# Optimization experiments

Hardware: AMD Instinct MI355X
Metric: run time of the kernel (lower is better)

Reference implementation:

```python
import jax, jax.numpy as jnp
import numpy as np

B, N, F_IN, F_OUT = 32, 1024, 64, 64
ALPHA = 0.2  # LeakyReLU negative slope


def setup_inputs() -> dict:
    key = jax.random.key(0)
    k1, k2, k3, k4 = jax.random.split(key, 4)
    node_features = jax.random.normal(k1, (B, N, F_IN), dtype=jnp.float32)
    adjacency = jax.random.uniform(k2, (B, N, N)) > 0.5
    adjacency = adjacency | jnp.eye(N, dtype=bool)[None]  # self-loops: no all-masked row
    # xavier_uniform-scale params (normal with matching std is fine for a reference)
    W = jax.random.normal(k3, (F_IN, F_OUT), dtype=jnp.float32) * (2.0 / (F_IN + F_OUT)) ** 0.5
    a = jax.random.normal(k4, (2 * F_OUT, 1), dtype=jnp.float32) * (2.0 / (2 * F_OUT + 1)) ** 0.5
    return {"node_features": node_features, "adjacency": adjacency, "W": W, "a": a}


def reference(node_features, adjacency, W, a):
    # h = X W : (B, N, F_OUT)
    h = node_features @ W
    # a^T [h_i || h_j] = h_i . a1 + h_j . a2  (exact decomposition of the concat score)
    a1 = a[:F_OUT, 0]
    a2 = a[F_OUT:, 0]
    f1 = jnp.einsum('bnf,f->bn', h, a1)  # (B, N)
    f2 = jnp.einsum('bnf,f->bn', h, a2)  # (B, N)
    e = jax.nn.leaky_relu(f1[:, :, None] + f2[:, None, :], negative_slope=ALPHA)  # (B,N,N)
    e = jnp.where(adjacency, e, -jnp.inf)
    attention = jax.nn.softmax(e, axis=-1)  # masked softmax over neighbors j
    h_prime = jnp.einsum('bij,bjf->bif', attention, h)  # (B, N, F_OUT)
    return jax.nn.elu(h_prime)  # concat=True branch
```

## Files before the change

kernel.cpp:

```cpp
#include <hip/hip_runtime.h>
#include <hip/hip_bf16.h>


#define B_  32
#define N_  1024
#define F_  64

typedef __attribute__((ext_vector_type(8))) short  short8;
typedef __attribute__((ext_vector_type(4))) float  floatx4;

__device__ __forceinline__ short f2bf(float x) {
    unsigned u = __float_as_uint(x);
    u += 0x7fff + ((u >> 16) & 1);
    return (short)(u >> 16);
}

__global__ __launch_bounds__(256) void gat_prep(
    const float* __restrict__ nf, const float* __restrict__ W, const float* __restrict__ a,
    float* __restrict__ f1, float* __restrict__ f2, short* __restrict__ h_swz)
{
    const int wave = threadIdx.x >> 6;
    const int lane = threadIdx.x & 63;
    const long long row0 = (long long)blockIdx.x * 16 + wave * 4;

    const float* nf0 = nf + row0 * F_;
    float acc0 = 0.f, acc1 = 0.f, acc2 = 0.f, acc3 = 0.f;
    #pragma unroll 8
    for (int k = 0; k < F_; ++k) {
        float wk = W[k * F_ + lane];
        acc0 = fmaf(nf0[k],          wk, acc0);
        acc1 = fmaf(nf0[F_ + k],     wk, acc1);
        acc2 = fmaf(nf0[2 * F_ + k], wk, acc2);
        acc3 = fmaf(nf0[3 * F_ + k], wk, acc3);
    }
    const float a1 = a[lane], a2 = a[F_ + lane];

    float accs[4] = {acc0, acc1, acc2, acc3};
    #pragma unroll
    for (int r = 0; r < 4; ++r) {
        float v  = accs[r];
        float s1 = v * a1, s2 = v * a2;
        #pragma unroll
        for (int off = 32; off >= 1; off >>= 1) {
            s1 += __shfl_xor(s1, off, 64);
            s2 += __shfl_xor(s2, off, 64);
        }
        long long row = row0 + r;
        if (lane == 0) { f1[row] = s1; f2[row] = s2; }
        int jl = (int)(row & (N_ - 1));
        int k  = jl & 31;
        int n  = lane & 15, fg = lane >> 4;
        int lp = n | ((k >> 3) << 4), e = k & 7;
        long long gc = row >> 5;
        h_swz[(gc * 4 + fg) * 512 + lp * 8 + e] = f2bf(v);
    }
}

__global__ __launch_bounds__(256) void gat_attn(
    const int* __restrict__ adj, const float* __restrict__ f1g, const float* __restrict__ f2g,
    const short* __restrict__ h_swz, float* __restrict__ out)
{
    const int wave = threadIdx.x >> 6;
    const int lane = threadIdx.x & 63;
    const int b  = blockIdx.x >> 4;
    const int ib = blockIdx.x & 15;
    const int i_base = ib * 64 + wave * 16;
    const int iw = lane & 15;
    const int kg = lane >> 4;
    const int i  = i_base + iw;

    const float f1i = f1g[b * N_ + i];
    const int*   adjrow = adj + ((long long)b * N_ + i) * N_ + kg * 8;
    const float* f2b    = f2g + b * N_ + kg * 8;
    const short* hb     = h_swz + (long long)b * 65536 + lane * 8;

    floatx4 acc0 = {0.f,0.f,0.f,0.f}, acc1 = {0.f,0.f,0.f,0.f};
    floatx4 acc2 = {0.f,0.f,0.f,0.f}, acc3 = {0.f,0.f,0.f,0.f};
    float s_lane = 0.f;

    for (int jc = 0; jc < 32; ++jc) {
        int4 aA = *(const int4*)(adjrow + jc * 32);
        int4 aB = *(const int4*)(adjrow + jc * 32 + 4);
        floatx4 fA = *(const floatx4*)(f2b + jc * 32);
        floatx4 fB = *(const floatx4*)(f2b + jc * 32 + 4);

        int   am[8] = {aA.x, aA.y, aA.z, aA.w, aB.x, aB.y, aB.z, aB.w};
        float fv[8] = {fA[0], fA[1], fA[2], fA[3], fB[0], fB[1], fB[2], fB[3]};

        short8 afrag;
        #pragma unroll
        for (int e = 0; e < 8; ++e) {
            float x  = f1i + fv[e];
            x        = fmaxf(x, 0.2f * x);
            float pe = am[e] ? __expf(x) : 0.f;
            s_lane  += pe;
            afrag[e] = f2bf(pe);
        }

        const short* hc = hb + jc * 2048;
        short8 b0 = *(const short8*)(hc);
        short8 b1 = *(const short8*)(hc + 512);
        short8 b2 = *(const short8*)(hc + 1024);
        short8 b3 = *(const short8*)(hc + 1536);

        acc0 = __builtin_amdgcn_mfma_f32_16x16x32_bf16(afrag, b0, acc0, 0, 0, 0);
        acc1 = __builtin_amdgcn_mfma_f32_16x16x32_bf16(afrag, b1, acc1, 0, 0, 0);
        acc2 = __builtin_amdgcn_mfma_f32_16x16x32_bf16(afrag, b2, acc2, 0, 0, 0);
        acc3 = __builtin_amdgcn_mfma_f32_16x16x32_bf16(afrag, b3, acc3, 0, 0, 0);
    }

    s_lane += __shfl_xor(s_lane, 16, 64);
    s_lane += __shfl_xor(s_lane, 32, 64);

    float* orow = out + ((long long)b * N_ + i_base) * F_;
    floatx4 accs[4] = {acc0, acc1, acc2, acc3};
    #pragma unroll
    for (int fg = 0; fg < 4; ++fg) {
        #pragma unroll
        for (int r = 0; r < 4; ++r) {
            int rloc = kg * 4 + r;
            float sr = __shfl(s_lane, rloc, 64);
            float v  = accs[fg][r] / sr;
            v = v > 0.f ? v : (__expf(v) - 1.f);
            orow[(long long)rloc * F_ + fg * 16 + iw] = v;
        }
    }
}

extern "C" void kernel_launch(void* const* d_in, const int* in_sizes, int n_in,
                              void* d_out, int out_size, void* d_ws, size_t ws_size,
                              hipStream_t stream) {
    const float* nf  = (const float*)d_in[0];
    const int*   adj = (const int*)d_in[1];
    const float* W   = (const float*)d_in[2];
    const float* a   = (const float*)d_in[3];
    float* out = (float*)d_out;

    char* ws = (char*)d_ws;
    float* f1    = (float*)ws;
    float* f2    = (float*)(ws + 131072);
    short* h_swz = (short*)(ws + 262144);

    hipLaunchKernelGGL(gat_prep, dim3(B_ * N_ / 16), dim3(256), 0, stream,
                       nf, W, a, f1, f2, h_swz);
    hipLaunchKernelGGL(gat_attn, dim3(B_ * (N_ / 64)), dim3(256), 0, stream,
                       adj, f1, f2, h_swz, out);
}
```

Baseline: 58.53 us.

## Split attention j-range across waves with shared-memory reduction of partial sums

Each block now handles 16 rows instead of 64, and its four waves each cover a quarter of the neighbor dimension. Partial MFMA accumulators and row sums go to LDS and are combined after a barrier, with each wave finishing one feature group. The grid grows fourfold to 2048 blocks, so more waves are in flight to hide latency on the adjacency stream. In exchange it adds LDS traffic and a __syncthreads, and the loads are reordered with an occupancy hint in the launch bounds.

```diff
diff --git a/kernel.cpp b/kernel.cpp
--- a/kernel.cpp
+++ b/kernel.cpp
@@ -56,52 +56,67 @@
     }
 }
 
-__global__ __launch_bounds__(256) void gat_attn(
+__global__ __launch_bounds__(256, 8) void gat_attn(
     const int* __restrict__ adj, const float* __restrict__ f1g, const float* __restrict__ f2g,
     const short* __restrict__ h_swz, float* __restrict__ out)
 {
+    __shared__ float part[4][64][17];
+    __shared__ float srow[4][16];
+
     const int wave = threadIdx.x >> 6;
     const int lane = threadIdx.x & 63;
-    const int b  = blockIdx.x >> 4;
-    const int ib = blockIdx.x & 15;
-    const int i_base = ib * 64 + wave * 16;
+    const int b  = blockIdx.x >> 6;
+    const int ig = blockIdx.x & 63;
+    const int i_base = ig * 16;
     const int iw = lane & 15;
     const int kg = lane >> 4;
     const int i  = i_base + iw;
+    const int j0 = wave * 256;
 
     const float f1i = f1g[b * N_ + i];
-    const int*   adjrow = adj + ((long long)b * N_ + i) * N_ + kg * 8;
-    const float* f2b    = f2g + b * N_ + kg * 8;
-    const short* hb     = h_swz + (long long)b * 65536 + lane * 8;
+    const int*   adjrow = adj + ((long long)b * N_ + i) * N_ + j0 + kg * 8;
+    const float* f2b    = f2g + b * N_ + j0 + kg * 8;
+    const short* hb     = h_swz + (long long)b * 65536 + wave * (8 * 2048) + lane * 8;
 
     floatx4 acc0 = {0.f,0.f,0.f,0.f}, acc1 = {0.f,0.f,0.f,0.f};
     floatx4 acc2 = {0.f,0.f,0.f,0.f}, acc3 = {0.f,0.f,0.f,0.f};
     float s_lane = 0.f;
 
-    for (int jc = 0; jc < 32; ++jc) {
+    for (int jc = 0; jc < 8; ++jc) {
         int4 aA = *(const int4*)(adjrow + jc * 32);
         int4 aB = *(const int4*)(adjrow + jc * 32 + 4);
         floatx4 fA = *(const floatx4*)(f2b + jc * 32);
         floatx4 fB = *(const floatx4*)(f2b + jc * 32 + 4);
-
-        int   am[8] = {aA.x, aA.y, aA.z, aA.w, aB.x, aB.y, aB.z, aB.w};
-        float fv[8] = {fA[0], fA[1], fA[2], fA[3], fB[0], fB[1], fB[2], fB[3]};
-
-        short8 afrag;
-        #pragma unroll
-        for (int e = 0; e < 8; ++e) {
-            float x  = f1i + fv[e];
-            x        = fmaxf(x, 0.2f * x);
-            float pe = am[e] ? __expf(x) : 0.f;
-            s_lane  += pe;
-            afrag[e] = f2bf(pe);
-        }
 
         const short* hc = hb + jc * 2048;
         short8 b0 = *(const short8*)(hc);
         short8 b1 = *(const short8*)(hc + 512);
         short8 b2 = *(const short8*)(hc + 1024);
         short8 b3 = *(const short8*)(hc + 1536);
+
+        short8 afrag;
+        {
+            int   am[4] = {aA.x, aA.y, aA.z, aA.w};
+            #pragma unroll
+            for (int e = 0; e < 4; ++e) {
+                float x  = f1i + fA[e];
+                x        = fmaxf(x, 0.2f * x);
+                float pe = am[e] ? __expf(x) : 0.f;
+                s_lane  += pe;
+                afrag[e] = f2bf(pe);
+            }
+        }
+        {
+            int   am[4] = {aB.x, aB.y, aB.z, aB.w};
+            #pragma unroll
+            for (int e = 0; e < 4; ++e) {
+                float x  = f1i + fB[e];
+                x        = fmaxf(x, 0.2f * x);
+                float pe = am[e] ? __expf(x) : 0.f;
+                s_lane  += pe;
+                afrag[e + 4] = f2bf(pe);
+            }
+        }
 
         acc0 = __builtin_amdgcn_mfma_f32_16x16x32_bf16(afrag, b0, acc0, 0, 0, 0);
         acc1 = __builtin_amdgcn_mfma_f32_16x16x32_bf16(afrag, b1, acc1, 0, 0, 0);
@@ -111,19 +126,28 @@
 
     s_lane += __shfl_xor(s_lane, 16, 64);
     s_lane += __shfl_xor(s_lane, 32, 64);
+    if (lane < 16) srow[wave][lane] = s_lane;
 
-    float* orow = out + ((long long)b * N_ + i_base) * F_;
     floatx4 accs[4] = {acc0, acc1, acc2, acc3};
     #pragma unroll
-    for (int fg = 0; fg < 4; ++fg) {
+    for (int fg = 0; fg < 4; ++fg)
         #pragma unroll
-        for (int r = 0; r < 4; ++r) {
-            int rloc = kg * 4 + r;
-            float sr = __shfl(s_lane, rloc, 64);
-            float v  = accs[fg][r] / sr;
-            v = v > 0.f ? v : (__expf(v) - 1.f);
-            orow[(long long)rloc * F_ + fg * 16 + iw] = v;
-        }
+        for (int r = 0; r < 4; ++r)
+            part[wave][lane][fg * 4 + r] = accs[fg][r];
+    __syncthreads();
+
+    const int fg = wave;
+    float* orow = out + ((long long)b * N_ + i_base) * F_;
+    #pragma unroll
+    for (int r = 0; r < 4; ++r) {
+        const int idx  = fg * 4 + r;
+        const int rloc = kg * 4 + r;
+        float tot  = part[0][lane][idx] + part[1][lane][idx]
+                   + part[2][lane][idx] + part[3][lane][idx];
+        float sden = srow[0][rloc] + srow[1][rloc] + srow[2][rloc] + srow[3][rloc];
+        float v = tot / sden;
+        v = v > 0.f ? v : (__expf(v) - 1.f);
+        orow[(long long)rloc * F_ + fg * 16 + iw] = v;
     }
 }
 
@@ -143,6 +167,6 @@
 
     hipLaunchKernelGGL(gat_prep, dim3(B_ * N_ / 16), dim3(256), 0, stream,
                        nf, W, a, f1, f2, h_swz);
-    hipLaunchKernelGGL(gat_attn, dim3(B_ * (N_ / 64)), dim3(256), 0, stream,
+    hipLaunchKernelGGL(gat_attn, dim3(B_ * (N_ / 16)), dim3(256), 0, stream,
                        adj, f1, f2, h_swz, out);
 }
```

Result: slower. 60.69 us (+3.7%).
